# Kernel tuning notes

Measured on AMD Instinct MI355X. Metric: run time of the kernel, lower is better.

Reference implementation:

```python
import jax, jax.numpy as jnp
import numpy as np

N_NODES = 100000
N_EDGES = 3200000
NFEAT, NHID, NCLASS = 512, 128, 40


def _glorot(key, fan_in, fan_out):
    lim = jnp.sqrt(6.0 / (fan_in + fan_out))
    return jax.random.uniform(key, (fan_in, fan_out), jnp.float32, -lim, lim)


def setup_inputs() -> dict:
    key = jax.random.key(0)
    k1, k2, k3, k4, k5 = jax.random.split(key, 5)
    x = jax.random.normal(k1, (N_NODES, NFEAT), jnp.float32)
    edge_index = jax.random.randint(k2, (2, N_EDGES), 0, N_NODES, jnp.int64)
    edge_weight = jax.random.uniform(k3, (N_EDGES,), jnp.float32)
    W1 = _glorot(k4, NFEAT, NHID)
    b1 = jnp.zeros((NHID,), jnp.float32)
    W2 = _glorot(k5, NHID, NCLASS)
    b2 = jnp.zeros((NCLASS,), jnp.float32)
    return {"x": x, "edge_index": edge_index, "edge_weight": edge_weight,
            "W1": W1, "b1": b1, "W2": W2, "b2": b2}


def _gcn_norm(edge_index, edge_weight, num_nodes):
    # add self loops (weight 1), symmetric normalization D^-1/2 A D^-1/2
    loop = jnp.arange(num_nodes, dtype=edge_index.dtype)
    row = jnp.concatenate([edge_index[0], loop])
    col = jnp.concatenate([edge_index[1], loop])
    w = jnp.concatenate([edge_weight, jnp.ones((num_nodes,), edge_weight.dtype)])
    deg = jax.ops.segment_sum(w, col, num_segments=num_nodes)
    dinv = jnp.where(deg > 0, jax.lax.rsqrt(jnp.maximum(deg, 1e-20)), 0.0)
    norm = dinv[row] * w * dinv[col]
    return row, col, norm


def _gcn_conv(h, row, col, norm, W, b, num_nodes):
    h = h @ W                                  # [N, out]
    msg = norm[:, None] * h[row]               # per-edge gather + scale
    out = jax.ops.segment_sum(msg, col, num_segments=num_nodes)  # scatter-add
    return out + b


def reference(x, edge_index, edge_weight, W1, b1, W2, b2):
    n = x.shape[0]
    row, col, norm = _gcn_norm(edge_index, edge_weight, n)
    h = jax.nn.relu(_gcn_conv(x, row, col, norm, W1, b1, n))
    # dropout: eval mode (training=False) -> identity
    return _gcn_conv(h, row, col, norm, W2, b2, n)
```

## Files before the change

### kernel.cpp

```cpp
#include <hip/hip_runtime.h>

#define NN 100000
#define NE 3200000
#define NF 512
#define NH 128
#define NC 40
#define NBIN 196
#define BINW 512
#define CAP  20480
#define EPB  4096

typedef __attribute__((ext_vector_type(8))) short bfrag;
typedef __attribute__((ext_vector_type(4))) float f32x4;
typedef __attribute__((ext_vector_type(8))) unsigned short u16x8;

static __device__ __forceinline__ unsigned short f2bf(float x) {
  unsigned u = __float_as_uint(x);
  u += 0x7FFF + ((u >> 16) & 1);
  return (unsigned short)(u >> 16);
}
static __device__ __forceinline__ float bf2f(unsigned short b) {
  return __uint_as_float(((unsigned)b) << 16);
}
static __device__ __forceinline__ float bflo(unsigned u) { return __uint_as_float(u << 16); }
static __device__ __forceinline__ float bfhi(unsigned u) { return __uint_as_float(u & 0xFFFF0000u); }


__global__ __launch_bounds__(256) void k_wconv(const float* __restrict__ W1,
                                               unsigned short* __restrict__ Wfh,
                                               unsigned short* __restrict__ Wfl,
                                               int* __restrict__ binfill) {
  if (blockIdx.x == 0 && threadIdx.x < NBIN) binfill[threadIdx.x] = 0;
  int i = blockIdx.x * 256 + threadIdx.x;
  int k = i >> 7, n = i & 127;
  float w = W1[i];
  unsigned short hi = f2bf(w);
  unsigned short lo = f2bf(w - bf2f(hi));
  int idx = ((k >> 3) * 128 + n) * 8 + (k & 7);
  Wfh[idx] = hi; Wfl[idx] = lo;
}


__global__ __launch_bounds__(256) void k_binA(const int* __restrict__ row, const int* __restrict__ col,
                                              const float* __restrict__ w,
                                              int* __restrict__ binfill, int2* __restrict__ binned) {
  __shared__ int hist[NBIN];
  __shared__ int base[NBIN];
  int t = threadIdx.x;
  int eb = blockIdx.x * EPB;
  for (int i = t; i < NBIN; i += 256) hist[i] = 0;
  __syncthreads();
  int rk[16], bn[16], sr[16]; float wv[16];
#pragma unroll
  for (int j = 0; j < 16; ++j) {
    int e = eb + t + j * 256;
    if (e < NE) {
      int c = __builtin_nontemporal_load(col + e);
      bn[j] = c >> 9;
      sr[j] = __builtin_nontemporal_load(row + e) | ((c & 511) << 17);
      wv[j] = __builtin_nontemporal_load(w + e);
      rk[j] = atomicAdd(&hist[bn[j]], 1);
    } else bn[j] = -1;
  }
  __syncthreads();
  if (t < NBIN) { int hv = hist[t]; base[t] = hv ? atomicAdd(&binfill[t], hv) : 0; }
  __syncthreads();
#pragma unroll
  for (int j = 0; j < 16; ++j) {
    if (bn[j] >= 0) {
      int pos = base[bn[j]] + rk[j];
      if (pos < CAP) binned[(size_t)bn[j] * CAP + pos] = make_int2(sr[j], __float_as_int(wv[j]));
    }
  }
}


__global__ __launch_bounds__(256) void k_binscan(const int* __restrict__ binfill,
                                                 int* __restrict__ binptr, int* __restrict__ rowptr) {
  __shared__ int sm[256];
  int t = threadIdx.x;
  sm[t] = (t < NBIN) ? binfill[t] : 0;
  __syncthreads();
  for (int off = 1; off < 256; off <<= 1) {
    int a = (t >= off) ? sm[t - off] : 0;
    __syncthreads();
    sm[t] += a;
    __syncthreads();
  }
  if (t <= NBIN) binptr[t] = (t == 0) ? 0 : sm[t - 1];
  if (t == 0) rowptr[NN] = NE;
}


__global__ __launch_bounds__(256) void k_binB(const int* __restrict__ binfill, const int* __restrict__ binptr,
                                              const int2* __restrict__ binned, int2* __restrict__ pair,
                                              int* __restrict__ rowptr, float* __restrict__ dinv) {
  __shared__ unsigned long long pk[BINW];
  __shared__ unsigned short lrank[CAP];
  __shared__ int lptr[BINW];
  __shared__ int sm[256];
  int t = threadIdx.x;
  int bin = blockIdx.x;
  int cnt = binfill[bin]; if (cnt > CAP) cnt = CAP;
  int bb = binptr[bin];
  pk[t] = 0ULL; pk[t + 256] = 0ULL;
  __syncthreads();
  const int2* src = binned + (size_t)bin * CAP;
  for (int i = t; i < cnt; i += 256) {
    int2 r = src[i];
    int lc = (unsigned)r.x >> 17;
    unsigned long long fw = (unsigned long long)(unsigned)(__int_as_float(r.y) * 16777216.0f + 0.5f);
    unsigned long long old = atomicAdd(&pk[lc], (1ULL << 42) | fw);
    lrank[i] = (unsigned short)(old >> 42);
  }
  __syncthreads();
  int c0 = (int)(pk[2 * t] >> 42), c1 = (int)(pk[2 * t + 1] >> 42);
  sm[t] = c0 + c1;
  __syncthreads();
  for (int off = 1; off < 256; off <<= 1) {
    int a = (t >= off) ? sm[t - off] : 0;
    __syncthreads();
    sm[t] += a;
    __syncthreads();
  }
  int excl = (t == 0) ? 0 : sm[t - 1];
  lptr[2 * t] = excl;
  lptr[2 * t + 1] = excl + c0;
  int n0 = bin * BINW + 2 * t;
  if (n0 < NN) {
    rowptr[n0] = bb + excl;
    float d = (float)(pk[2 * t] & 0x3FFFFFFFFFFULL) * (1.0f / 16777216.0f) + 1.0f;
    dinv[n0] = rsqrtf(d);
  }
  if (n0 + 1 < NN) {
    rowptr[n0 + 1] = bb + excl + c0;
    float d = (float)(pk[2 * t + 1] & 0x3FFFFFFFFFFULL) * (1.0f / 16777216.0f) + 1.0f;
    dinv[n0 + 1] = rsqrtf(d);
  }
  __syncthreads();
  for (int i = t; i < cnt; i += 256) {
    int2 r = src[i];
    int lc = (unsigned)r.x >> 17;
    int pos = bb + lptr[lc] + (int)lrank[i];
    pair[pos] = make_int2(r.x & 0x1FFFF, r.y);
  }
}


__global__ __launch_bounds__(256) void k_gemm1(const float* __restrict__ X,
                                               const unsigned short* __restrict__ Wfh,
                                               const unsigned short* __restrict__ Wfl,
                                               const float* __restrict__ dinv,
                                               unsigned short* __restrict__ HXb) {
  __shared__ unsigned short Ah[2048], Bh[4096], Bl[4096];
  int t = threadIdx.x;
  int lane = t & 63;
  int wid = t >> 6;
  int m0 = blockIdx.x * 64;
  int srow = t >> 2;
  int quad = t & 3;
  const float* xrow = X + (size_t)(m0 + srow) * NF + quad * 8;
  bool mok = (m0 + srow) < NN;
  int wm = wid >> 1, wn = wid & 1;
  int mb = wm * 32, nb = wn * 64;
  int fr = lane & 15, fg = lane >> 4;

  f32x4 acc[2][4];
#pragma unroll
  for (int i = 0; i < 2; ++i)
#pragma unroll
    for (int j = 0; j < 4; ++j) acc[i][j] = (f32x4)0.0f;

  for (int ks = 0; ks < 16; ++ks) {
    const u16x8* sh = (const u16x8*)(Wfh + (size_t)ks * 4096);
    const u16x8* sl = (const u16x8*)(Wfl + (size_t)ks * 4096);
    u16x8 b0 = sh[t], b1 = sh[t + 256];
    u16x8 c0 = sl[t], c1 = sl[t + 256];
    float4 xv0 = mok ? *(const float4*)(xrow + ks * 32)     : make_float4(0.f, 0.f, 0.f, 0.f);
    float4 xv1 = mok ? *(const float4*)(xrow + ks * 32 + 4) : make_float4(0.f, 0.f, 0.f, 0.f);
#pragma unroll
    for (int q = 0; q < 2; ++q) {
      float4 xq = q ? xv1 : xv0;
      float f[4] = {xq.x, xq.y, xq.z, xq.w};
      unsigned short h[4];
#pragma unroll
      for (int j = 0; j < 4; ++j) h[j] = f2bf(f[j]);
      int base = (quad * 64 + srow) * 8 + q * 4;
      uint2 hv = make_uint2((unsigned)h[0] | ((unsigned)h[1] << 16),
                            (unsigned)h[2] | ((unsigned)h[3] << 16));
      *(uint2*)&Ah[base] = hv;
    }
    ((u16x8*)Bh)[t] = b0; ((u16x8*)Bh)[t + 256] = b1;
    ((u16x8*)Bl)[t] = c0; ((u16x8*)Bl)[t + 256] = c1;
    __syncthreads();
    bfrag ah[2], bh[4], bl[4];
#pragma unroll
    for (int mi = 0; mi < 2; ++mi)
      ah[mi] = *(bfrag*)&Ah[(fg * 64 + mb + mi * 16 + fr) * 8];
#pragma unroll
    for (int nt = 0; nt < 4; ++nt) {
      int idx = (fg * 128 + nb + nt * 16 + fr) * 8;
      bh[nt] = *(bfrag*)&Bh[idx];
      bl[nt] = *(bfrag*)&Bl[idx];
    }
#pragma unroll
    for (int mi = 0; mi < 2; ++mi)
#pragma unroll
      for (int nt = 0; nt < 4; ++nt) {
        acc[mi][nt] = __builtin_amdgcn_mfma_f32_16x16x32_bf16(ah[mi], bh[nt], acc[mi][nt], 0, 0, 0);
        acc[mi][nt] = __builtin_amdgcn_mfma_f32_16x16x32_bf16(ah[mi], bl[nt], acc[mi][nt], 0, 0, 0);
      }
    __syncthreads();
  }
#pragma unroll
  for (int mi = 0; mi < 2; ++mi) {
    int rb = m0 + mb + mi * 16 + fg * 4;
#pragma unroll
    for (int q = 0; q < 4; ++q) {
      int r = rb + q;
      if (r < NN) {
        float dv = dinv[r];
#pragma unroll
        for (int nt = 0; nt < 4; ++nt) {
          int c = nb + nt * 16 + fr;
          __builtin_nontemporal_store(f2bf(dv * acc[mi][nt][q]), HXb + (size_t)r * NH + c);
        }
      }
    }
  }
}


#define FMA8(n, v)                                            \
  { unsigned uu[4] = {(v).x, (v).y, (v).z, (v).w};            \
    _Pragma("unroll")                                         \
    for (int q = 0; q < 4; ++q) {                             \
      ax[q] = fmaf((n), bflo(uu[q]), ax[q]);                  \
      ay[q] = fmaf((n), bfhi(uu[q]), ay[q]);                  \
    } }

__global__ __launch_bounds__(256) void k_agg1(const int* __restrict__ rowptr, const int2* __restrict__ pair,
                                              const unsigned* __restrict__ hxb, const float* __restrict__ dinv,
                                              const float* __restrict__ b1, unsigned* __restrict__ hb) {
  int wid = (blockIdx.x * 256 + threadIdx.x) >> 6;
  int lane = threadIdx.x & 63;
  if (wid >= NN) return;
  int sub = lane >> 4, fl = lane & 15;
  int beg = rowptr[wid], end = rowptr[wid + 1];
  const uint4* hx4 = (const uint4*)hxb;
  const long long* pr = (const long long*)pair;
  float ax[4] = {0.f, 0.f, 0.f, 0.f}, ay[4] = {0.f, 0.f, 0.f, 0.f};
  int e = beg;
  for (; e + 16 <= end; e += 16) {
    long long r0 = pr[e + sub];
    long long r1 = pr[e + 4 + sub];
    long long r2 = pr[e + 8 + sub];
    long long r3 = pr[e + 12 + sub];
    uint4 v0 = hx4[(size_t)(unsigned)(r0 & 0x1FFFF) * 16 + fl];
    uint4 v1 = hx4[(size_t)(unsigned)(r1 & 0x1FFFF) * 16 + fl];
    uint4 v2 = hx4[(size_t)(unsigned)(r2 & 0x1FFFF) * 16 + fl];
    uint4 v3 = hx4[(size_t)(unsigned)(r3 & 0x1FFFF) * 16 + fl];
    float n0 = __int_as_float((int)(r0 >> 32));
    float n1 = __int_as_float((int)(r1 >> 32));
    float n2 = __int_as_float((int)(r2 >> 32));
    float n3 = __int_as_float((int)(r3 >> 32));
    FMA8(n0, v0);
    FMA8(n1, v1);
    FMA8(n2, v2);
    FMA8(n3, v3);
  }
  for (; e + 8 <= end; e += 8) {
    long long r0 = pr[e + sub];
    long long r1 = pr[e + 4 + sub];
    uint4 v0 = hx4[(size_t)(unsigned)(r0 & 0x1FFFF) * 16 + fl];
    uint4 v1 = hx4[(size_t)(unsigned)(r1 & 0x1FFFF) * 16 + fl];
    float n0 = __int_as_float((int)(r0 >> 32));
    float n1 = __int_as_float((int)(r1 >> 32));
    FMA8(n0, v0);
    FMA8(n1, v1);
  }
  for (; e < end; e += 4) {
    int idx = e + sub;
    bool ok = idx < end;
    long long r0 = ok ? pr[idx] : 0;
    unsigned s = ok ? (unsigned)(r0 & 0x1FFFF) : (unsigned)wid;
    float n0 = ok ? __int_as_float((int)(r0 >> 32)) : 0.f;
    uint4 v0 = hx4[(size_t)s * 16 + fl];
    FMA8(n0, v0);
  }
  if (sub == 0) {
    uint4 ov = hx4[(size_t)wid * 16 + fl];
    FMA8(1.0f, ov);
  }
#pragma unroll
  for (int q = 0; q < 4; ++q) {
    ax[q] += __shfl_xor(ax[q], 16, 64); ay[q] += __shfl_xor(ay[q], 16, 64);
    ax[q] += __shfl_xor(ax[q], 32, 64); ay[q] += __shfl_xor(ay[q], 32, 64);
  }
  if (sub == 0) {
    float di = dinv[wid];
    float4 bA = ((const float4*)b1)[fl * 2];
    float4 bB = ((const float4*)b1)[fl * 2 + 1];
    float bxs[4] = {bA.x, bA.z, bB.x, bB.z};
    float bys[4] = {bA.y, bA.w, bB.y, bB.w};
    unsigned o[4];
#pragma unroll
    for (int q = 0; q < 4; ++q) {
      float rx = fmaxf(fmaf(di, ax[q], bxs[q]), 0.f);
      float ry = fmaxf(fmaf(di, ay[q], bys[q]), 0.f);
      o[q] = (unsigned)f2bf(rx) | ((unsigned)f2bf(ry) << 16);
    }
    ((uint4*)hb)[(size_t)wid * 16 + fl] = make_uint4(o[0], o[1], o[2], o[3]);
  }
}


__global__ __launch_bounds__(256) void k_gemm2(const unsigned* __restrict__ hb, const float* __restrict__ W2,
                                               const float* __restrict__ dinv,
                                               unsigned short* __restrict__ H2b) {
  __shared__ float Hs[32][132];
  __shared__ float Ws[NH * NC];
  int t = threadIdx.x;
  int m0 = blockIdx.x * 32;
  {
    int r = t >> 3, cb = (t & 7) * 8;
    int rowi = m0 + r;
    if (rowi < NN) {
      uint4 a = *(const uint4*)(hb + (size_t)rowi * 64 + cb);
      uint4 b = *(const uint4*)(hb + (size_t)rowi * 64 + cb + 4);
      unsigned u[8] = {a.x, a.y, a.z, a.w, b.x, b.y, b.z, b.w};
#pragma unroll
      for (int j = 0; j < 8; ++j) {
        Hs[r][cb * 2 + j * 2]     = bflo(u[j]);
        Hs[r][cb * 2 + j * 2 + 1] = bfhi(u[j]);
      }
    } else {
#pragma unroll
      for (int j = 0; j < 16; ++j) Hs[r][cb * 2 + j] = 0.f;
    }
  }
  for (int i = t; i < NH * NC; i += 256) Ws[i] = W2[i];
  __syncthreads();
  int r = t >> 3, c0 = (t & 7) * 5;
  float acc[5] = {0.f, 0.f, 0.f, 0.f, 0.f};
#pragma unroll 4
  for (int k = 0; k < NH; ++k) {
    float hv = Hs[r][k];
#pragma unroll
    for (int j = 0; j < 5; ++j) acc[j] = fmaf(hv, Ws[k * NC + c0 + j], acc[j]);
  }
  int rowi = m0 + r;
  if (rowi < NN) {
    float dv = dinv[rowi];
#pragma unroll
    for (int j = 0; j < 5; ++j)
      __builtin_nontemporal_store(f2bf(dv * acc[j]), H2b + (size_t)rowi * 64 + c0 + j);
    int prr = t & 7;
    if (prr < 3) {
#pragma unroll
      for (int j = 0; j < 8; ++j)
        __builtin_nontemporal_store((unsigned short)0, H2b + (size_t)rowi * 64 + 40 + prr * 8 + j);
    }
  }
}


#define FMA4(n, v)                                            \
  { unsigned uu[2] = {(v).x, (v).y};                          \
    _Pragma("unroll")                                         \
    for (int q = 0; q < 2; ++q) {                             \
      ax[q] = fmaf((n), bflo(uu[q]), ax[q]);                  \
      ay[q] = fmaf((n), bfhi(uu[q]), ay[q]);                  \
    } }

__global__ __launch_bounds__(256) void k_agg2(const int* __restrict__ rowptr, const int2* __restrict__ pair,
                                              const unsigned* __restrict__ h2u,
                                              const float* __restrict__ dinv,
                                              const float* __restrict__ b2, float* __restrict__ out) {
  int wid = (blockIdx.x * 256 + threadIdx.x) >> 6;
  int lane = threadIdx.x & 63;
  if (wid >= NN) return;
  int sub = lane >> 4, fl = lane & 15;
  int beg = rowptr[wid], end = rowptr[wid + 1];
  const uint2* h4 = (const uint2*)h2u;
  const long long* pr = (const long long*)pair;
  float ax[2] = {0.f, 0.f}, ay[2] = {0.f, 0.f};
  int e = beg;
  for (; e + 16 <= end; e += 16) {
    long long r0 = pr[e + sub];
    long long r1 = pr[e + 4 + sub];
    long long r2 = pr[e + 8 + sub];
    long long r3 = pr[e + 12 + sub];
    uint2 v0 = h4[(size_t)(unsigned)(r0 & 0x1FFFF) * 16 + fl];
    uint2 v1 = h4[(size_t)(unsigned)(r1 & 0x1FFFF) * 16 + fl];
    uint2 v2 = h4[(size_t)(unsigned)(r2 & 0x1FFFF) * 16 + fl];
    uint2 v3 = h4[(size_t)(unsigned)(r3 & 0x1FFFF) * 16 + fl];
    float n0 = __int_as_float((int)(r0 >> 32));
    float n1 = __int_as_float((int)(r1 >> 32));
    float n2 = __int_as_float((int)(r2 >> 32));
    float n3 = __int_as_float((int)(r3 >> 32));
    FMA4(n0, v0);
    FMA4(n1, v1);
    FMA4(n2, v2);
    FMA4(n3, v3);
  }
  for (; e + 8 <= end; e += 8) {
    long long r0 = pr[e + sub];
    long long r1 = pr[e + 4 + sub];
    uint2 v0 = h4[(size_t)(unsigned)(r0 & 0x1FFFF) * 16 + fl];
    uint2 v1 = h4[(size_t)(unsigned)(r1 & 0x1FFFF) * 16 + fl];
    float n0 = __int_as_float((int)(r0 >> 32));
    float n1 = __int_as_float((int)(r1 >> 32));
    FMA4(n0, v0);
    FMA4(n1, v1);
  }
  for (; e < end; e += 4) {
    int idx = e + sub;
    bool ok = idx < end;
    long long r0 = ok ? pr[idx] : 0;
    unsigned s = ok ? (unsigned)(r0 & 0x1FFFF) : (unsigned)wid;
    float n0 = ok ? __int_as_float((int)(r0 >> 32)) : 0.f;
    uint2 v0 = h4[(size_t)s * 16 + fl];
    FMA4(n0, v0);
  }
  if (sub == 0) {
    uint2 ov = h4[(size_t)wid * 16 + fl];
    FMA4(1.0f, ov);
  }
#pragma unroll
  for (int q = 0; q < 2; ++q) {
    ax[q] += __shfl_xor(ax[q], 16, 64); ay[q] += __shfl_xor(ay[q], 16, 64);
    ax[q] += __shfl_xor(ax[q], 32, 64); ay[q] += __shfl_xor(ay[q], 32, 64);
  }
  if (sub == 0 && fl < 10) {
    float di = dinv[wid];
    float4 bv = ((const float4*)b2)[fl];
    float4 o = make_float4(fmaf(di, ax[0], bv.x), fmaf(di, ay[0], bv.y),
                           fmaf(di, ax[1], bv.z), fmaf(di, ay[1], bv.w));
    *(float4*)(out + (size_t)wid * NC + fl * 4) = o;
  }
}


extern "C" void kernel_launch(void* const* d_in, const int* in_sizes, int n_in,
                              void* d_out, int out_size, void* d_ws, size_t ws_size,
                              hipStream_t stream) {
  const float* x  = (const float*)d_in[0];
  const int*   ei = (const int*)d_in[1];
  const float* ew = (const float*)d_in[2];
  const float* W1 = (const float*)d_in[3];
  const float* b1 = (const float*)d_in[4];
  const float* W2 = (const float*)d_in[5];
  const float* b2 = (const float*)d_in[6];
  float* out = (float*)d_out;
  const int* row = ei;
  const int* col = ei + NE;

  char* ws = (char*)d_ws;
  size_t o = 0;
  auto alloc = [&](size_t bytes) -> void* {
    void* p = ws + o;
    o += (bytes + 255) & ~(size_t)255;
    return p;
  };
  float* dinv    = (float*)alloc((size_t)NN * 4);
  int*   rowptr  = (int*)alloc((size_t)(NN + 1) * 4);
  int*   binfill = (int*)alloc(1024);
  int*   binptr  = (int*)alloc(1024);
  int2*  pair    = (int2*)alloc((size_t)NE * 8);
  unsigned short* Wfh = (unsigned short*)alloc((size_t)NF * NH * 2);
  unsigned short* Wfl = (unsigned short*)alloc((size_t)NF * NH * 2);
  unsigned short* hxb = (unsigned short*)alloc((size_t)NN * NH * 2);
  unsigned*       hb  = (unsigned*)alloc((size_t)NN * NH * 2);
  int2*  binned  = (int2*)alloc((size_t)NBIN * CAP * 8);
  unsigned short* h2b = (unsigned short*)hxb;

  k_wconv<<<(NF * NH) / 256, 256, 0, stream>>>(W1, Wfh, Wfl, binfill);
  k_binA<<<(NE + EPB - 1) / EPB, 256, 0, stream>>>(row, col, ew, binfill, binned);
  k_binscan<<<1, 256, 0, stream>>>(binfill, binptr, rowptr);
  k_binB<<<NBIN, 256, 0, stream>>>(binfill, binptr, binned, pair, rowptr, dinv);
  k_gemm1<<<(NN + 63) / 64, 256, 0, stream>>>(x, Wfh, Wfl, dinv, hxb);
  k_agg1<<<(NN * 64) / 256, 256, 0, stream>>>(rowptr, pair, (const unsigned*)hxb, dinv, b1, hb);
  k_gemm2<<<(NN + 31) / 32, 256, 0, stream>>>(hb, W2, dinv, h2b);
  k_agg2<<<(NN * 64) / 256, 256, 0, stream>>>(rowptr, pair, (const unsigned*)h2b, dinv, b2, out);
}
```

Before: 386.6 us.

## Stage half of each X row tile in LDS per phase with wide contiguous loads

The first GEMM now loads and converts 256 columns of each 64-row X tile into a 32 KB LDS buffer in two phases, instead of fetching 32 floats per k-step. Each thread issues 16 contiguous float4 loads per phase covering a 64-float span, which gives more memory-level parallelism and longer contiguous reads from the streamed 200 MB X matrix. The B-fragment k-loop then reads A from the staged buffer. The cost is much larger LDS use per block, which may lower occupancy, plus extra barriers.

```diff
diff --git a/kernel.cpp b/kernel.cpp
--- a/kernel.cpp
+++ b/kernel.cpp
@@ -152,18 +152,19 @@
                                                const unsigned short* __restrict__ Wfl,
                                                const float* __restrict__ dinv,
                                                unsigned short* __restrict__ HXb) {
-  __shared__ unsigned short Ah[2048], Bh[4096], Bl[4096];
+  __shared__ unsigned short Ah[16384];
+  __shared__ unsigned short Bh[4096], Bl[4096];
   int t = threadIdx.x;
   int lane = t & 63;
   int wid = t >> 6;
   int m0 = blockIdx.x * 64;
-  int srow = t >> 2;
-  int quad = t & 3;
-  const float* xrow = X + (size_t)(m0 + srow) * NF + quad * 8;
+  int srow = t >> 2, quad = t & 3;
+  const float* xrow = X + (size_t)(m0 + srow) * NF;
   bool mok = (m0 + srow) < NN;
   int wm = wid >> 1, wn = wid & 1;
   int mb = wm * 32, nb = wn * 64;
   int fr = lane & 15, fg = lane >> 4;
+  const float4 z4 = make_float4(0.f, 0.f, 0.f, 0.f);
 
   f32x4 acc[2][4];
 #pragma unroll
@@ -171,46 +172,55 @@
 #pragma unroll
     for (int j = 0; j < 4; ++j) acc[i][j] = (f32x4)0.0f;
 
-  for (int ks = 0; ks < 16; ++ks) {
-    const u16x8* sh = (const u16x8*)(Wfh + (size_t)ks * 4096);
-    const u16x8* sl = (const u16x8*)(Wfl + (size_t)ks * 4096);
-    u16x8 b0 = sh[t], b1 = sh[t + 256];
-    u16x8 c0 = sl[t], c1 = sl[t + 256];
-    float4 xv0 = mok ? *(const float4*)(xrow + ks * 32)     : make_float4(0.f, 0.f, 0.f, 0.f);
-    float4 xv1 = mok ? *(const float4*)(xrow + ks * 32 + 4) : make_float4(0.f, 0.f, 0.f, 0.f);
-#pragma unroll
-    for (int q = 0; q < 2; ++q) {
-      float4 xq = q ? xv1 : xv0;
-      float f[4] = {xq.x, xq.y, xq.z, xq.w};
-      unsigned short h[4];
-#pragma unroll
-      for (int j = 0; j < 4; ++j) h[j] = f2bf(f[j]);
-      int base = (quad * 64 + srow) * 8 + q * 4;
-      uint2 hv = make_uint2((unsigned)h[0] | ((unsigned)h[1] << 16),
-                            (unsigned)h[2] | ((unsigned)h[3] << 16));
-      *(uint2*)&Ah[base] = hv;
-    }
-    ((u16x8*)Bh)[t] = b0; ((u16x8*)Bh)[t + 256] = b1;
-    ((u16x8*)Bl)[t] = c0; ((u16x8*)Bl)[t + 256] = c1;
-    __syncthreads();
-    bfrag ah[2], bh[4], bl[4];
-#pragma unroll
-    for (int mi = 0; mi < 2; ++mi)
-      ah[mi] = *(bfrag*)&Ah[(fg * 64 + mb + mi * 16 + fr) * 8];
-#pragma unroll
-    for (int nt = 0; nt < 4; ++nt) {
-      int idx = (fg * 128 + nb + nt * 16 + fr) * 8;
-      bh[nt] = *(bfrag*)&Bh[idx];
-      bl[nt] = *(bfrag*)&Bl[idx];
-    }
-#pragma unroll
-    for (int mi = 0; mi < 2; ++mi)
+  for (int ph = 0; ph < 2; ++ph) {
+    if (ph) __syncthreads();
+#pragma unroll
+    for (int b = 0; b < 2; ++b) {
+      float4 xv[8];
+#pragma unroll
+      for (int c = 0; c < 8; ++c) {
+        int k = ph * 256 + quad * 64 + b * 32 + c * 4;
+        xv[c] = mok ? *(const float4*)(xrow + k) : z4;
+      }
+#pragma unroll
+      for (int c = 0; c < 8; ++c) {
+        int kl = quad * 64 + b * 32 + c * 4;
+        int kchunk = kl >> 3;
+        int pos = (kchunk * 64 + srow) * 8 + (kl & 7);
+        unsigned short h0 = f2bf(xv[c].x), h1 = f2bf(xv[c].y);
+        unsigned short h2 = f2bf(xv[c].z), h3 = f2bf(xv[c].w);
+        *(uint2*)&Ah[pos] = make_uint2((unsigned)h0 | ((unsigned)h1 << 16),
+                                       (unsigned)h2 | ((unsigned)h3 << 16));
+      }
+    }
+    for (int kss = 0; kss < 8; ++kss) {
+      int ks = ph * 8 + kss;
+      const u16x8* sh = (const u16x8*)(Wfh + (size_t)ks * 4096);
+      const u16x8* sl = (const u16x8*)(Wfl + (size_t)ks * 4096);
+      u16x8 b0 = sh[t], b1 = sh[t + 256];
+      u16x8 c0 = sl[t], c1 = sl[t + 256];
+      __syncthreads();
+      ((u16x8*)Bh)[t] = b0; ((u16x8*)Bh)[t + 256] = b1;
+      ((u16x8*)Bl)[t] = c0; ((u16x8*)Bl)[t + 256] = c1;
+      __syncthreads();
+      bfrag ah[2], bh[4], bl[4];
+#pragma unroll
+      for (int mi = 0; mi < 2; ++mi)
+        ah[mi] = *(bfrag*)&Ah[((kss * 4 + fg) * 64 + mb + mi * 16 + fr) * 8];
 #pragma unroll
       for (int nt = 0; nt < 4; ++nt) {
-        acc[mi][nt] = __builtin_amdgcn_mfma_f32_16x16x32_bf16(ah[mi], bh[nt], acc[mi][nt], 0, 0, 0);
-        acc[mi][nt] = __builtin_amdgcn_mfma_f32_16x16x32_bf16(ah[mi], bl[nt], acc[mi][nt], 0, 0, 0);
+        int idx = (fg * 128 + nb + nt * 16 + fr) * 8;
+        bh[nt] = *(bfrag*)&Bh[idx];
+        bl[nt] = *(bfrag*)&Bl[idx];
       }
-    __syncthreads();
+#pragma unroll
+      for (int mi = 0; mi < 2; ++mi)
+#pragma unroll
+        for (int nt = 0; nt < 4; ++nt) {
+          acc[mi][nt] = __builtin_amdgcn_mfma_f32_16x16x32_bf16(ah[mi], bh[nt], acc[mi][nt], 0, 0, 0);
+          acc[mi][nt] = __builtin_amdgcn_mfma_f32_16x16x32_bf16(ah[mi], bl[nt], acc[mi][nt], 0, 0, 0);
+        }
+    }
   }
 #pragma unroll
   for (int mi = 0; mi < 2; ++mi) {
```

Result: slower. 481.6 us (+24.6%).
